# Kernel optimization log

Hardware: AMD Instinct MI355X
Metric: run time of the kernel (lower is better)

## Reference

```python
import jax, jax.numpy as jnp
import numpy as np

V, E, R, D, OUT, B = 50000, 400000, 400, 100, 200, 1024
EPS = 1e-5


def ccorr(a, b):
    # circular correlation: irfft(conj(rfft(a)) * rfft(b), n=D)
    return jnp.fft.irfft(jnp.conj(jnp.fft.rfft(a)) * jnp.fft.rfft(b), n=a.shape[-1]).astype(a.dtype)


def setup_inputs() -> dict:
    key = jax.random.key(0)
    ks = jax.random.split(key, 16)
    xav = lambda k, shp: jax.random.normal(k, shp, dtype=jnp.float32) * np.sqrt(2.0 / (shp[0] + shp[-1])) * np.sqrt(2.0)
    return {
        # graph / query (int constants)
        "edge_src": jax.random.randint(ks[0], (E,), 0, V, dtype=jnp.int32),
        "edge_dst": jax.random.randint(ks[1], (E,), 0, V, dtype=jnp.int32),
        "edge_type": jax.random.randint(ks[2], (E,), 0, R, dtype=jnp.int32),
        "head": jax.random.randint(ks[3], (B,), 0, V, dtype=jnp.int32),
        "rela": jax.random.randint(ks[4], (B,), 0, R, dtype=jnp.int32),
        "edge_norm": jax.random.uniform(ks[5], (E,), dtype=jnp.float32),
        # learned parameters
        "ent_emb": xav(ks[6], (V, D)),
        "rel_emb": xav(ks[7], (R, D)),
        "in_w": xav(ks[8], (D, OUT)),
        "out_w": xav(ks[9], (D, OUT)),
        "loop_w": xav(ks[10], (D, OUT)),
        "w_rel": xav(ks[11], (D, OUT)),
        "loop_rel": xav(ks[12], (1, D)),
        "conv_bias": jnp.zeros((OUT,), jnp.float32),
        "bn_gamma": jnp.ones((OUT,), jnp.float32),
        "bn_beta": jnp.zeros((OUT,), jnp.float32),
        "emb_ent": xav(ks[13], (V, OUT)),
        "ent_bias": jnp.zeros((V,), jnp.float32),
    }


def reference(edge_src, edge_dst, edge_type, head, rela, edge_norm,
              ent_emb, rel_emb, in_w, out_w, loop_w, w_rel, loop_rel,
              conv_bias, bn_gamma, bn_beta, emb_ent, ent_bias):
    # --- CompGCNCov (eval mode: dropouts are identity) ---
    h_src = ent_emb[edge_src]          # [E, D] gather
    r_e = rel_emb[edge_type]           # [E, D] gather
    edge_data = ccorr(h_src, r_e)      # [E, D] FFT compose (opn='corr')
    half = E // 2
    msg = jnp.concatenate([edge_data[:half] @ in_w, edge_data[half:] @ out_w])  # [E, OUT]
    msg = msg * edge_norm[:, None]
    agg = jax.ops.segment_sum(msg, edge_dst, num_segments=V) / 3.0             # scatter-sum + /3
    loop = ccorr(ent_emb, jnp.broadcast_to(loop_rel, ent_emb.shape)) @ loop_w / 3.0
    x = agg + loop + conv_bias
    # BatchNorm1d with batch statistics (training-mode stats, affine)
    mean = x.mean(axis=0)
    var = x.var(axis=0)
    x = (x - mean) / jnp.sqrt(var + EPS) * bn_gamma + bn_beta
    x = jnp.tanh(x)                    # act
    r_out = rel_emb @ w_rel            # [R, OUT]
    # --- DistMult decoder ---
    head_emb = x[head]                 # [B, OUT]
    rela_emb = r_out[rela]             # [B, OUT]
    obj = head_emb * rela_emb
    score = jax.nn.sigmoid(obj @ emb_ent.T + ent_bias)  # [B, V]
    return score
```

## Files before the change

### kernel.cpp

```cpp
#include <hip/hip_runtime.h>
#include <cstddef>

constexpr int V = 50000, E = 400000, R = 400, D = 100, OUT = 200, B = 1024;
constexpr int HALF = E / 2;
constexpr float EPS = 1e-5f;
constexpr int K2 = 232;
constexpr int VPAD = 50176;
constexpr int NKEY = 800;
constexpr int E1MAX = 450560;
constexpr int MT_O = 208, MT_K = 128;
constexpr int MT_SZ = MT_O * MT_K;
constexpr int NB2 = 196;
constexpr int BCAP = 2560;
constexpr int ECHK = 8;

typedef short bf16x8 __attribute__((ext_vector_type(8)));
typedef float f32x4  __attribute__((ext_vector_type(4)));
typedef unsigned short ushort8 __attribute__((ext_vector_type(8)));
typedef __attribute__((address_space(1))) const unsigned int guint_t;
typedef __attribute__((address_space(3))) unsigned int luint_t;

__device__ inline unsigned short f2bf(float x) {
    unsigned u = __float_as_uint(x);
    u = (u + 0x7fffu + ((u >> 16) & 1u)) >> 16;
    return (unsigned short)u;
}
__device__ inline float bf2f(unsigned short u) {
    return __uint_as_float(((unsigned)u) << 16);
}

constexpr int G_MLOOP = (D * OUT + 255) / 256;
constexpr int G_ROUT  = (R * OUT + 255) / 256;
constexpr int G_CVTWT = (2 * 208 * 16) / 256;
constexpr int G_CVTENT = (V * 16) / 256;
constexpr int PRE_B1 = G_MLOOP;
constexpr int PRE_B2 = PRE_B1 + G_ROUT;
constexpr int PRE_B3 = PRE_B2 + G_CVTWT;
constexpr int PRE_NWG = PRE_B3 + G_CVTENT;

__global__ __launch_bounds__(256) void k_pre(const float* __restrict__ loop_rel,
                                             const float* __restrict__ loop_w,
                                             const float* __restrict__ rel_emb,
                                             const float* __restrict__ w_rel,
                                             const float* __restrict__ in_w,
                                             const float* __restrict__ out_w,
                                             const float* __restrict__ ent_emb,
                                             float* __restrict__ Mloop,
                                             float* __restrict__ r_out,
                                             unsigned short* __restrict__ WT_bf,
                                             unsigned short* __restrict__ ent_bf) {
    int blk = blockIdx.x, t = threadIdx.x;
    if (blk < PRE_B1) {
        int i = blk * 256 + t;
        if (i >= D * OUT) return;
        int j = i / OUT, o = i % OUT;
        float s = 0.f;
        for (int k = 0; k < D; ++k) {
            int idx = j + k; if (idx >= D) idx -= D;
            s += loop_rel[idx] * loop_w[k * OUT + o];
        }
        Mloop[i] = s;
    } else if (blk < PRE_B2) {
        int i = (blk - PRE_B1) * 256 + t;
        if (i >= R * OUT) return;
        int r = i / OUT, o = i % OUT;
        float s = 0.f;
        for (int k = 0; k < D; ++k) s += rel_emb[r * D + k] * w_rel[k * OUT + o];
        r_out[i] = s;
    } else if (blk < PRE_B3) {
        int i = (blk - PRE_B2) * 256 + t;
        int side = i / (208 * 16);
        int rem = i - side * 208 * 16;
        int o = rem >> 4, c8 = rem & 15;
        int k0 = c8 * 8;
        const float* __restrict__ W = side ? out_w : in_w;
        ushort8 v = (ushort8)0;
        if (o < 200) {
#pragma unroll
            for (int q = 0; q < 8; ++q) {
                int k = k0 + q;
                if (k < 100) v[q] = f2bf(W[k * OUT + o]);
            }
        }
        *(ushort8*)&WT_bf[((size_t)side * 208 + o) * 128 + k0] = v;
    } else {
        int i = (blk - PRE_B3) * 256 + t;
        if (i >= V * 16) return;
        int v = i >> 4, c8 = i & 15;
        int c0 = c8 * 8;
        ushort8 o = (ushort8)0;
        if (c0 < 96) {
            float4 f0 = *(const float4*)&ent_emb[(size_t)v * D + c0];
            float4 f1 = *(const float4*)&ent_emb[(size_t)v * D + c0 + 4];
            o[0] = f2bf(f0.x); o[1] = f2bf(f0.y); o[2] = f2bf(f0.z); o[3] = f2bf(f0.w);
            o[4] = f2bf(f1.x); o[5] = f2bf(f1.y); o[6] = f2bf(f1.z); o[7] = f2bf(f1.w);
        } else if (c0 == 96) {
            float4 f0 = *(const float4*)&ent_emb[(size_t)v * D + 96];
            o[0] = f2bf(f0.x); o[1] = f2bf(f0.y); o[2] = f2bf(f0.z); o[3] = f2bf(f0.w);
        }
        *(ushort8*)&ent_bf[(size_t)v * 128 + c0] = o;
    }
}

__global__ __launch_bounds__(256) void k_hist(const int* __restrict__ etyp,
                                              int* __restrict__ hist1) {
    __shared__ int lh[NKEY];
    int t = threadIdx.x;
    for (int i = t; i < NKEY; i += 256) lh[i] = 0;
    __syncthreads();
    for (int e = blockIdx.x * 256 + t; e < E; e += gridDim.x * 256) {
        int key = etyp[e] + (e < HALF ? 0 : R);
        atomicAdd(&lh[key], 1);
    }
    __syncthreads();
    for (int i = t; i < NKEY; i += 256) {
        int c = lh[i];
        if (c) atomicAdd(&hist1[i], c);
    }
}

__global__ __launch_bounds__(1024) void k_scan(const int* __restrict__ hist1,
                                               int* __restrict__ start1,
                                               int* __restrict__ Edev) {
    __shared__ int buf[1024];
    int t = threadIdx.x;
    int c = (t < NKEY) ? ((hist1[t] + 63) & ~63) : 0;
    buf[t] = c; __syncthreads();
    for (int off = 1; off < 1024; off <<= 1) {
        int x = (t >= off) ? buf[t - off] : 0; __syncthreads();
        buf[t] += x; __syncthreads();
    }
    if (t < NKEY) start1[t] = buf[t] - c;
    if (t == NKEY - 1) { start1[NKEY] = buf[t]; *Edev = buf[t]; }
}

__global__ __launch_bounds__(1024) void k_binkey(const int* __restrict__ etyp,
                                                 const int* __restrict__ start1,
                                                 int* __restrict__ cursor1,
                                                 unsigned* __restrict__ perm1,
                                                 int* __restrict__ pos_of_e) {
    __shared__ int lhist[NKEY], lbase[NKEY], lcnt[NKEY];
    int t = threadIdx.x;
    int e0 = blockIdx.x * 8192;
    for (int i = t; i < NKEY; i += 1024) { lhist[i] = 0; lcnt[i] = 0; }
    __syncthreads();
    for (int i = t; i < 8192; i += 1024) {
        int e = e0 + i;
        if (e < E) {
            int key = etyp[e] + (e < HALF ? 0 : R);
            atomicAdd(&lhist[key], 1);
        }
    }
    __syncthreads();
    for (int i = t; i < NKEY; i += 1024) {
        int c = lhist[i];
        lbase[i] = c ? (start1[i] + atomicAdd(&cursor1[i], c)) : 0;
    }
    __syncthreads();
    for (int i = t; i < 8192; i += 1024) {
        int e = e0 + i;
        if (e < E) {
            int key = etyp[e] + (e < HALF ? 0 : R);
            int r = atomicAdd(&lcnt[key], 1);
            int p = lbase[key] + r;
            perm1[p] = (unsigned)e | ((unsigned)key << 19);
            pos_of_e[e] = p;
        }
    }
}

__global__ __launch_bounds__(1024) void k_bindst1(const int* __restrict__ edst,
                                                  const int* __restrict__ pos_of_e,
                                                  int* __restrict__ cursor196,
                                                  uint2* __restrict__ pairs) {
    __shared__ int chist[NB2], cbase[NB2], ccnt[NB2];
    int t = threadIdx.x;
    int e0 = blockIdx.x * 8192;
    for (int i = t; i < NB2; i += 1024) { chist[i] = 0; ccnt[i] = 0; }
    __syncthreads();
    for (int i = t; i < 8192; i += 1024) {
        int e = e0 + i;
        if (e < E) atomicAdd(&chist[edst[e] >> 8], 1);
    }
    __syncthreads();
    for (int i = t; i < NB2; i += 1024) {
        int c = chist[i];
        cbase[i] = c ? atomicAdd(&cursor196[i], c) : 0;
    }
    __syncthreads();
    for (int i = t; i < 8192; i += 1024) {
        int e = e0 + i;
        if (e < E) {
            int d = edst[e];
            int ld = d >> 8;
            int r = atomicAdd(&ccnt[ld], 1);
            int slot = cbase[ld] + r;
            if (slot < BCAP)
                pairs[(size_t)ld * BCAP + slot] = make_uint2((unsigned)d, (unsigned)pos_of_e[e]);
        }
    }
}

__global__ __launch_bounds__(256) void k_bindst2(const int* __restrict__ cursor196,
                                                 const uint2* __restrict__ pairs,
                                                 int* __restrict__ start2,
                                                 int* __restrict__ poslist) {
    __shared__ int lcnt[256], loff[256], lrk[256], bscan[256];
    int b = blockIdx.x, t = threadIdx.x;
    lcnt[t] = 0; lrk[t] = 0;
    bscan[t] = (t < NB2) ? min(cursor196[t], BCAP) : 0;
    __syncthreads();
    for (int off = 1; off < 256; off <<= 1) {
        int xx = (t >= off) ? bscan[t - off] : 0; __syncthreads();
        bscan[t] += xx; __syncthreads();
    }
    int base = (b > 0) ? bscan[b - 1] : 0;
    if (b == 0 && t == 0) start2[V] = bscan[NB2 - 1];
    int n = min(cursor196[b], BCAP);
    for (int i = t; i < n; i += 256) {
        int d = (int)pairs[(size_t)b * BCAP + i].x;
        atomicAdd(&lcnt[d - (b << 8)], 1);
    }
    __syncthreads();
    int cc = lcnt[t];
    loff[t] = cc; __syncthreads();
    for (int off = 1; off < 256; off <<= 1) {
        int xx = (t >= off) ? loff[t - off] : 0; __syncthreads();
        loff[t] += xx; __syncthreads();
    }
    int excl = loff[t] - cc;
    loff[t] = excl;
    int d = (b << 8) + t;
    if (d < V) start2[d] = base + excl;
    __syncthreads();
    for (int i = t; i < n; i += 256) {
        uint2 pr = pairs[(size_t)b * BCAP + i];
        int ld = (int)pr.x - (b << 8);
        int r = atomicAdd(&lrk[ld], 1);
        poslist[base + loff[ld] + r] = (int)pr.y;
    }
}

__global__ __launch_bounds__(256) void k_mtab(const float* __restrict__ rel_emb,
                                              const unsigned short* __restrict__ WT_bf,
                                              unsigned short* __restrict__ Mtab) {
    __shared__ unsigned short rsh[256];
    int key = blockIdx.x;
    int rho = (key < R) ? key : key - R;
    int side = (key < R) ? 0 : 1;
    int t = threadIdx.x, lane = t & 63, wid = t >> 6;
    {
        int sm = t;
        if (sm >= 200) sm -= 200; else if (sm >= 100) sm -= 100;
        rsh[t] = f2bf(rel_emb[rho * D + sm]);
    }
    __syncthreads();
    const unsigned short* WT = WT_bf + (size_t)side * 208 * 128;
    unsigned short* MtK = Mtab + (size_t)key * MT_SZ;
    int m16 = lane & 15, kq = lane >> 4;
    for (int jt = 0; jt < 2; ++jt) {
        int j0 = (wid * 2 + jt) * 16;
        f32x4 acc[13] = {};
        for (int ks = 0; ks < 4; ++ks) {
            int rbase = ks * 32 + kq * 8 + j0 + m16;
            ushort8 tmp;
#pragma unroll
            for (int q = 0; q < 8; ++q) tmp[q] = rsh[rbase + q];
            bf16x8 bfr = *(bf16x8*)&tmp;
#pragma unroll
            for (int of = 0; of < 13; ++of) {
                bf16x8 afr = *(const bf16x8*)&WT[(size_t)(of * 16 + m16) * 128 + ks * 32 + kq * 8];
                acc[of] = __builtin_amdgcn_mfma_f32_16x16x32_bf16(afr, bfr, acc[of], 0, 0, 0);
            }
        }
#pragma unroll
        for (int of = 0; of < 13; ++of) {
            int orow = of * 16 + kq * 4;
#pragma unroll
            for (int q = 0; q < 4; ++q)
                MtK[(size_t)(orow + q) * MT_K + j0 + m16] = f2bf(acc[of][q]);
        }
    }
}

__global__ __launch_bounds__(256, 2) void k_edgemm(const unsigned* __restrict__ perm1,
                                                   const int* __restrict__ Edev,
                                                   const int* __restrict__ esrc,
                                                   const float* __restrict__ enorm,
                                                   const unsigned short* __restrict__ ent_bf,
                                                   const unsigned short* __restrict__ Mtab,
                                                   unsigned short* __restrict__ msg) {
    __shared__ __align__(16) unsigned short MtL[MT_SZ];
    __shared__ __align__(16) unsigned short AtL[64 * MT_K];
    __shared__ float snrm[2][64];
    __shared__ int ssrc[2][64];
    int t = threadIdx.x, lane = t & 63, wid = t >> 6;
    int cpx = gridDim.x >> 3;
    int blk = (blockIdx.x & 7) * cpx + (blockIdx.x >> 3);
    int nE = *Edev;
    int curkey = -1;
    for (int c = 0; c < ECHK; ++c) {
        int chunk = blk * ECHK + c;
        if (chunk * 64 >= nE) break;
        int buf = c & 1;
        if (t < 64) {
            unsigned val = perm1[chunk * 64 + t];
            int e = (int)(val & 0x7FFFFu);
            bool ok = (val != 0xFFFFFFFFu);
            ssrc[buf][t] = ok ? esrc[e] : 0;
            snrm[buf][t] = ok ? enorm[e] : 0.f;
        }
        int key = (int)(perm1[chunk * 64] >> 19);
        __syncthreads();
        if (key != curkey) {
            for (int i = 0; i < 13; ++i) {
                int G0 = (wid * 13 + i) * 64;
                int G = G0 + lane;
                int o = G >> 4, g = G & 15;
                int gs = g ^ (o & 7);
                __builtin_amdgcn_global_load_lds(
                    (guint_t*)(Mtab + (size_t)key * MT_SZ + o * MT_K + gs * 8),
                    (luint_t*)(MtL + (size_t)G0 * 8), 16, 0, 0);
            }
            curkey = key;
        }
        for (int i = 0; i < 4; ++i) {
            int base = (wid * 4 + i) * 1024;
            int Gb = base + lane * 16;
            int row = Gb >> 8;
            int g = (Gb >> 4) & 15;
            int gs = g ^ (row & 7);
            __builtin_amdgcn_global_load_lds(
                (guint_t*)(ent_bf + (size_t)ssrc[buf][row] * 128 + gs * 8),
                (luint_t*)((char*)AtL + base), 16, 0, 0);
        }
        __syncthreads();
        int erow = wid * 16 + (lane & 15);
        int kq = lane >> 4;
        f32x4 acc[13] = {};
        for (int ks = 0; ks < 4; ++ks) {
            int g = ks * 4 + kq;
            bf16x8 bfr = *(const bf16x8*)((const char*)AtL + erow * 256 + ((g ^ (erow & 7)) * 16));
#pragma unroll
            for (int of = 0; of < 13; ++of) {
                int orow = of * 16 + (lane & 15);
                bf16x8 afr = *(const bf16x8*)((const char*)MtL + orow * 256 + ((g ^ (orow & 7)) * 16));
                acc[of] = __builtin_amdgcn_mfma_f32_16x16x32_bf16(afr, bfr, acc[of], 0, 0, 0);
            }
        }
        float nr = snrm[buf][erow];
        size_t rowbase = (size_t)(chunk * 64 + erow) * OUT;
#pragma unroll
        for (int of = 0; of < 13; ++of) {
            int o0 = of * 16 + kq * 4;
            if (o0 < OUT) {
                ushort4 pk;
                pk.x = f2bf(acc[of][0] * nr); pk.y = f2bf(acc[of][1] * nr);
                pk.z = f2bf(acc[of][2] * nr); pk.w = f2bf(acc[of][3] * nr);
                *(ushort4*)&msg[rowbase + o0] = pk;
            }
        }
    }
}

__global__ __launch_bounds__(256) void k_aggx(const int* __restrict__ start2,
                                              const int* __restrict__ poslist,
                                              const unsigned short* __restrict__ msg,
                                              const float* __restrict__ ent_emb,
                                              const float* __restrict__ Mloop,
                                              const float* __restrict__ conv_bias,
                                              float* __restrict__ x) {
    __shared__ float xt[16][200];
    __shared__ float sat[100][20];
    int t = threadIdx.x, lane = t & 63, wid = t >> 6;
    int v0 = blockIdx.x * 16;
    int half = (lane >= 25 && lane < 50) ? 1 : 0;
    int c = lane - half * 25;
    bool act = lane < 50;
    int src = lane + 25 < 64 ? lane + 25 : 63;
    for (int i = 0; i < 4; ++i) {
        int v = v0 + wid * 4 + i;
        int s = start2[v], epos = start2[v + 1];
        float acc[8] = {};
        for (int q = s; q < epos; q += 2) {
            int qq = q + half;
            if (act && qq < epos) {
                int p = poslist[qq];
                ushort8 m = *(const ushort8*)&msg[(size_t)p * OUT + c * 8];
#pragma unroll
                for (int j = 0; j < 8; ++j) acc[j] += bf2f(m[j]);
            }
        }
#pragma unroll
        for (int j = 0; j < 8; ++j) {
            float o = __shfl(acc[j], src);
            if (lane < 25) acc[j] += o;
        }
        if (lane < 25) {
#pragma unroll
            for (int j = 0; j < 8; ++j) xt[wid * 4 + i][lane * 8 + j] = acc[j];
        }
    }
    for (int i = t; i < 400; i += 256) {
        int kg = i >> 4, vv = i & 15;
        float4 a4 = *(const float4*)&ent_emb[(size_t)(v0 + vv) * D + kg * 4];
        sat[kg * 4 + 0][vv] = a4.x;
        sat[kg * 4 + 1][vv] = a4.y;
        sat[kg * 4 + 2][vv] = a4.z;
        sat[kg * 4 + 3][vv] = a4.w;
    }
    __syncthreads();
    if (t < 200) {
        int og = t % 50, eg = t / 50;
        int o0 = og * 4, vv0 = eg * 4;
        float acc[4][4] = {};
        for (int k = 0; k < D; ++k) {
            float4 w4 = *(const float4*)&Mloop[k * OUT + o0];
            float4 ca = *(const float4*)&sat[k][vv0];
            float cc[4] = {ca.x, ca.y, ca.z, ca.w};
            float wv[4] = {w4.x, w4.y, w4.z, w4.w};
#pragma unroll
            for (int r = 0; r < 4; ++r)
#pragma unroll
                for (int j = 0; j < 4; ++j) acc[r][j] += cc[r] * wv[j];
        }
        float4 bi = *(const float4*)&conv_bias[o0];
        float bv[4] = {bi.x, bi.y, bi.z, bi.w};
#pragma unroll
        for (int r = 0; r < 4; ++r) {
            int vv = vv0 + r;
            float4 ov;
            ov.x = (xt[vv][o0 + 0] + acc[r][0]) * (1.f / 3.f) + bv[0];
            ov.y = (xt[vv][o0 + 1] + acc[r][1]) * (1.f / 3.f) + bv[1];
            ov.z = (xt[vv][o0 + 2] + acc[r][2]) * (1.f / 3.f) + bv[2];
            ov.w = (xt[vv][o0 + 3] + acc[r][3]) * (1.f / 3.f) + bv[3];
            *(float4*)&x[(size_t)(v0 + vv) * OUT + o0] = ov;
        }
    }
}

__global__ __launch_bounds__(256) void k_stats(const float* __restrict__ x,
                                               float* __restrict__ colsum,
                                               float* __restrict__ colsq) {
    int g = blockIdx.x * 256 + threadIdx.x;
    int col = g % OUT;
    int r0 = g / OUT;
    float s = 0.f, sq = 0.f;
    for (int r = r0; r < V; r += 512) {
        float v = x[(size_t)r * OUT + col];
        s += v;
        sq += v * v;
    }
    atomicAdd(&colsum[col], s);
    atomicAdd(&colsq[col], sq);
}

__global__ __launch_bounds__(256) void k_obj(const int* __restrict__ head,
                                             const int* __restrict__ rela,
                                             const float* __restrict__ x,
                                             const float* __restrict__ colsum,
                                             const float* __restrict__ colsq,
                                             const float* __restrict__ gamma,
                                             const float* __restrict__ beta,
                                             const float* __restrict__ r_out,
                                             unsigned short* __restrict__ obj_bf) {
    int b = blockIdx.x, t = threadIdx.x;
    if (t >= K2) return;
    float v = 0.f;
    if (t < OUT) {
        float m = colsum[t] / (float)V;
        float var = colsq[t] / (float)V - m * m;
        float rs = rsqrtf(var + EPS);
        int h = head[b], r = rela[b];
        float val = (x[(size_t)h * OUT + t] - m) * rs * gamma[t] + beta[t];
        val = tanhf(val);
        v = val * r_out[r * OUT + t];
    }
    obj_bf[(size_t)b * K2 + t] = f2bf(v);
}

__global__ __launch_bounds__(256) void k_cvt_emb(const float* __restrict__ emb_ent,
                                                 unsigned short* __restrict__ emb_bf) {
    int i = blockIdx.x * 256 + threadIdx.x;
    if (i >= VPAD * 29) return;
    int v = i / 29, c8 = i % 29;
    int c0 = c8 * 8;
    ushort8 o = (ushort8)0;
    if (v < V && c0 < 200) {
        float4 f0 = *(const float4*)&emb_ent[(size_t)v * OUT + c0];
        float4 f1 = *(const float4*)&emb_ent[(size_t)v * OUT + c0 + 4];
        o[0] = f2bf(f0.x); o[1] = f2bf(f0.y); o[2] = f2bf(f0.z); o[3] = f2bf(f0.w);
        o[4] = f2bf(f1.x); o[5] = f2bf(f1.y); o[6] = f2bf(f1.z); o[7] = f2bf(f1.w);
    }
    *(ushort8*)&emb_bf[(size_t)v * K2 + c0] = o;
}

constexpr int DEC_BM = 64, DEC_BN = 256;
constexpr int DEC_GX = B / DEC_BM;
constexpr int DEC_GY = VPAD / DEC_BN;
constexpr int DEC_NWG = DEC_GX * DEC_GY;

__global__ __launch_bounds__(256) void k_dec2(const unsigned short* __restrict__ obj_bf,
                                              const unsigned short* __restrict__ emb_bf,
                                              const float* __restrict__ ent_bias,
                                              float* __restrict__ score) {
    int t = threadIdx.x;
    int lane = t & 63, wid = t >> 6;
    int wg = (blockIdx.x & 7) * (DEC_NWG >> 3) + (blockIdx.x >> 3);
    int b0 = (wg & (DEC_GX - 1)) * DEC_BM;
    int v0 = (wg >> 4) * DEC_BN;
    int r16 = lane & 15;
    int kc = (lane >> 4) * 8;
    int vbase = v0 + wid * 64;
    const unsigned short* gA = obj_bf + (size_t)(b0 + r16) * K2 + kc;
    const unsigned short* gB = emb_bf + (size_t)(vbase + r16) * K2 + kc;
    f32x4 acc[4][4] = {};
    for (int ks = 0; ks < 7; ++ks) {
        int kof = ks * 32;
        bf16x8 a[4], bb[4];
#pragma unroll
        for (int mf = 0; mf < 4; ++mf)
            a[mf] = *(const bf16x8*)(gA + (size_t)(mf * 16) * K2 + kof);
#pragma unroll
        for (int nf = 0; nf < 4; ++nf)
            bb[nf] = *(const bf16x8*)(gB + (size_t)(nf * 16) * K2 + kof);
#pragma unroll
        for (int mf = 0; mf < 4; ++mf)
#pragma unroll
            for (int nf = 0; nf < 4; ++nf)
                acc[mf][nf] = __builtin_amdgcn_mfma_f32_16x16x32_bf16(a[mf], bb[nf],
                                                                      acc[mf][nf], 0, 0, 0);
    }
#pragma unroll
    for (int nf = 0; nf < 4; ++nf) {
        int v = vbase + nf * 16 + r16;
        if (v >= V) continue;
        float bias = ent_bias[v];
#pragma unroll
        for (int mf = 0; mf < 4; ++mf) {
            int brow = b0 + mf * 16 + (lane >> 4) * 4;
            f32x4 av = acc[mf][nf];
#pragma unroll
            for (int i = 0; i < 4; ++i) {
                float val = av[i] + bias;
                score[(size_t)(brow + i) * V + v] = 1.f / (1.f + __expf(-val));
            }
        }
    }
}

extern "C" void kernel_launch(void* const* d_in, const int* in_sizes, int n_in,
                              void* d_out, int out_size, void* d_ws, size_t ws_size,
                              hipStream_t stream) {
    const int*   edge_src  = (const int*)d_in[0];
    const int*   edge_dst  = (const int*)d_in[1];
    const int*   edge_type = (const int*)d_in[2];
    const int*   head      = (const int*)d_in[3];
    const int*   rela      = (const int*)d_in[4];
    const float* edge_norm = (const float*)d_in[5];
    const float* ent_emb   = (const float*)d_in[6];
    const float* rel_emb   = (const float*)d_in[7];
    const float* in_w      = (const float*)d_in[8];
    const float* out_w     = (const float*)d_in[9];
    const float* loop_w    = (const float*)d_in[10];
    const float* w_rel     = (const float*)d_in[11];
    const float* loop_rel  = (const float*)d_in[12];
    const float* conv_bias = (const float*)d_in[13];
    const float* bn_gamma  = (const float*)d_in[14];
    const float* bn_beta   = (const float*)d_in[15];
    const float* emb_ent   = (const float*)d_in[16];
    const float* ent_bias  = (const float*)d_in[17];
    float* score = (float*)d_out;

    char* w = (char*)d_ws;
    float*          agg    = (float*)w;                      w += (size_t)V * OUT * 4;
    unsigned short* Mtab   = (unsigned short*)w;             w += (size_t)NKEY * MT_SZ * 2;
    unsigned*       perm1  = (unsigned*)w;                   w += (size_t)E1MAX * 4;
    int*            pos_of_e = (int*)w;                      w += (size_t)E * 4;
    int*            poslist  = (int*)w;                      w += (size_t)E * 4;
    uint2*          pairs    = (uint2*)w;                    w += (size_t)NB2 * BCAP * 8;
    char* zbase = w;
    int*   hist1     = (int*)w;                              w += NKEY * 4;
    int*   cursor1   = (int*)w;                              w += NKEY * 4;
    int*   cursor196 = (int*)w;                              w += NB2 * 4;
    float* colsum    = (float*)w;                            w += OUT * 4;
    float* colsq     = (float*)w;                            w += OUT * 4;
    size_t zbytes = (size_t)(w - zbase);
    int*   start1  = (int*)w;                                w += (NKEY + 1) * 4;
    int*   start2  = (int*)w;                                w += (V + 4) * 4;
    int*   Edev    = (int*)w;                                w += 16;
    float* Mloop   = (float*)w;                              w += (size_t)D * OUT * 4;
    float* r_out   = (float*)w;                              w += (size_t)R * OUT * 4;
    unsigned short* obj_bf = (unsigned short*)w;             w += (size_t)B * K2 * 2;
    unsigned short* WT_bf  = (unsigned short*)w;             w += (size_t)2 * 208 * 128 * 2;
    unsigned short* ent_bf = (unsigned short*)agg;
    unsigned short* emb_bf = (unsigned short*)agg;
    unsigned short* msg    = (unsigned short*)d_out;

    hipMemsetAsync(zbase, 0, zbytes, stream);
    hipMemsetAsync(perm1, 0xFF, (size_t)E1MAX * 4, stream);

    k_hist<<<512, 256, 0, stream>>>(edge_type, hist1);
    k_scan<<<1, 1024, 0, stream>>>(hist1, start1, Edev);
    k_binkey<<<(E + 8191) / 8192, 1024, 0, stream>>>(edge_type, start1, cursor1,
                                                     perm1, pos_of_e);
    k_bindst1<<<(E + 8191) / 8192, 1024, 0, stream>>>(edge_dst, pos_of_e, cursor196, pairs);
    k_bindst2<<<NB2, 256, 0, stream>>>(cursor196, pairs, start2, poslist);
    k_pre<<<PRE_NWG, 256, 0, stream>>>(loop_rel, loop_w, rel_emb, w_rel, in_w, out_w,
                                       ent_emb, Mloop, r_out, WT_bf, ent_bf);
    k_mtab<<<NKEY, 256, 0, stream>>>(rel_emb, WT_bf, Mtab);
    k_edgemm<<<E1MAX / 64 / ECHK, 256, 0, stream>>>(perm1, Edev, edge_src, edge_norm,
                                                    ent_bf, Mtab, msg);
    k_aggx<<<V / 16, 256, 0, stream>>>(start2, poslist, msg, ent_emb, Mloop,
                                       conv_bias, agg);
    k_stats<<<400, 256, 0, stream>>>(agg, colsum, colsq);
    k_obj<<<B, 256, 0, stream>>>(head, rela, agg, colsum, colsq, bn_gamma, bn_beta,
                                 r_out, obj_bf);
    k_cvt_emb<<<(VPAD * 29 + 255) / 256, 256, 0, stream>>>(emb_ent, emb_bf);
    k_dec2<<<DEC_NWG, 256, 0, stream>>>(obj_bf, emb_bf, ent_bias, score);
}
```

Measured before the change: 413.7 us.

## Fuse binning kernels, pad perm in scan, convert emb_ent inside decoder

Measured after the change: 488.3 us. 18.0% more time.

```diff
diff --git a/kernel.cpp b/kernel.cpp
--- a/kernel.cpp
+++ b/kernel.cpp
@@ -1,4 +1,5 @@
 #include <hip/hip_runtime.h>
+#include <hip/hip_bf16.h>
 #include <cstddef>
 
 constexpr int V = 50000, E = 400000, R = 400, D = 100, OUT = 200, B = 1024;
@@ -27,6 +28,16 @@
 }
 __device__ inline float bf2f(unsigned short u) {
     return __uint_as_float(((unsigned)u) << 16);
+}
+__device__ inline unsigned short f2bfh(float x) {
+    __hip_bfloat16 h = __float2bfloat16(x);
+    return *reinterpret_cast<unsigned short*>(&h);
+}
+__device__ inline bf16x8 pack8(float4 f0, float4 f1) {
+    union { bf16x8 v; unsigned short u[8]; } r;
+    r.u[0] = f2bfh(f0.x); r.u[1] = f2bfh(f0.y); r.u[2] = f2bfh(f0.z); r.u[3] = f2bfh(f0.w);
+    r.u[4] = f2bfh(f1.x); r.u[5] = f2bfh(f1.y); r.u[6] = f2bfh(f1.z); r.u[7] = f2bfh(f1.w);
+    return r.v;
 }
 
 constexpr int G_MLOOP = (D * OUT + 255) / 256;
@@ -121,40 +132,55 @@
 
 __global__ __launch_bounds__(1024) void k_scan(const int* __restrict__ hist1,
                                                int* __restrict__ start1,
-                                               int* __restrict__ Edev) {
+                                               int* __restrict__ Edev,
+                                               unsigned* __restrict__ perm1) {
     __shared__ int buf[1024];
     int t = threadIdx.x;
-    int c = (t < NKEY) ? ((hist1[t] + 63) & ~63) : 0;
+    int h = (t < NKEY) ? hist1[t] : 0;
+    int c = (h + 63) & ~63;
     buf[t] = c; __syncthreads();
     for (int off = 1; off < 1024; off <<= 1) {
         int x = (t >= off) ? buf[t - off] : 0; __syncthreads();
         buf[t] += x; __syncthreads();
     }
-    if (t < NKEY) start1[t] = buf[t] - c;
+    int s = buf[t] - c;
+    if (t < NKEY) {
+        start1[t] = s;
+        for (int i = h; i < c; ++i) perm1[s + i] = 0xFFFFFFFFu;
+    }
     if (t == NKEY - 1) { start1[NKEY] = buf[t]; *Edev = buf[t]; }
 }
 
-__global__ __launch_bounds__(1024) void k_binkey(const int* __restrict__ etyp,
-                                                 const int* __restrict__ start1,
-                                                 int* __restrict__ cursor1,
-                                                 unsigned* __restrict__ perm1,
-                                                 int* __restrict__ pos_of_e) {
+__global__ __launch_bounds__(1024) void k_bin(const int* __restrict__ etyp,
+                                              const int* __restrict__ edst,
+                                              const int* __restrict__ start1,
+                                              int* __restrict__ cursor1,
+                                              int* __restrict__ cursor196,
+                                              unsigned* __restrict__ perm1,
+                                              uint2* __restrict__ pairs) {
     __shared__ int lhist[NKEY], lbase[NKEY], lcnt[NKEY];
+    __shared__ int chist[NB2], cbase[NB2], ccnt[NB2];
     int t = threadIdx.x;
     int e0 = blockIdx.x * 8192;
     for (int i = t; i < NKEY; i += 1024) { lhist[i] = 0; lcnt[i] = 0; }
+    for (int i = t; i < NB2; i += 1024) { chist[i] = 0; ccnt[i] = 0; }
     __syncthreads();
     for (int i = t; i < 8192; i += 1024) {
         int e = e0 + i;
         if (e < E) {
             int key = etyp[e] + (e < HALF ? 0 : R);
             atomicAdd(&lhist[key], 1);
+            atomicAdd(&chist[edst[e] >> 8], 1);
         }
     }
     __syncthreads();
     for (int i = t; i < NKEY; i += 1024) {
         int c = lhist[i];
         lbase[i] = c ? (start1[i] + atomicAdd(&cursor1[i], c)) : 0;
+    }
+    for (int i = t; i < NB2; i += 1024) {
+        int c = chist[i];
+        cbase[i] = c ? atomicAdd(&cursor196[i], c) : 0;
     }
     __syncthreads();
     for (int i = t; i < 8192; i += 1024) {
@@ -164,39 +190,12 @@
             int r = atomicAdd(&lcnt[key], 1);
             int p = lbase[key] + r;
             perm1[p] = (unsigned)e | ((unsigned)key << 19);
-            pos_of_e[e] = p;
-        }
-    }
-}
-
-__global__ __launch_bounds__(1024) void k_bindst1(const int* __restrict__ edst,
-                                                  const int* __restrict__ pos_of_e,
-                                                  int* __restrict__ cursor196,
-                                                  uint2* __restrict__ pairs) {
-    __shared__ int chist[NB2], cbase[NB2], ccnt[NB2];
-    int t = threadIdx.x;
-    int e0 = blockIdx.x * 8192;
-    for (int i = t; i < NB2; i += 1024) { chist[i] = 0; ccnt[i] = 0; }
-    __syncthreads();
-    for (int i = t; i < 8192; i += 1024) {
-        int e = e0 + i;
-        if (e < E) atomicAdd(&chist[edst[e] >> 8], 1);
-    }
-    __syncthreads();
-    for (int i = t; i < NB2; i += 1024) {
-        int c = chist[i];
-        cbase[i] = c ? atomicAdd(&cursor196[i], c) : 0;
-    }
-    __syncthreads();
-    for (int i = t; i < 8192; i += 1024) {
-        int e = e0 + i;
-        if (e < E) {
             int d = edst[e];
             int ld = d >> 8;
-            int r = atomicAdd(&ccnt[ld], 1);
-            int slot = cbase[ld] + r;
+            int rr = atomicAdd(&ccnt[ld], 1);
+            int slot = cbase[ld] + rr;
             if (slot < BCAP)
-                pairs[(size_t)ld * BCAP + slot] = make_uint2((unsigned)d, (unsigned)pos_of_e[e]);
+                pairs[(size_t)ld * BCAP + slot] = make_uint2((unsigned)d, (unsigned)p);
         }
     }
 }
@@ -479,29 +478,13 @@
     obj_bf[(size_t)b * K2 + t] = f2bf(v);
 }
 
-__global__ __launch_bounds__(256) void k_cvt_emb(const float* __restrict__ emb_ent,
-                                                 unsigned short* __restrict__ emb_bf) {
-    int i = blockIdx.x * 256 + threadIdx.x;
-    if (i >= VPAD * 29) return;
-    int v = i / 29, c8 = i % 29;
-    int c0 = c8 * 8;
-    ushort8 o = (ushort8)0;
-    if (v < V && c0 < 200) {
-        float4 f0 = *(const float4*)&emb_ent[(size_t)v * OUT + c0];
-        float4 f1 = *(const float4*)&emb_ent[(size_t)v * OUT + c0 + 4];
-        o[0] = f2bf(f0.x); o[1] = f2bf(f0.y); o[2] = f2bf(f0.z); o[3] = f2bf(f0.w);
-        o[4] = f2bf(f1.x); o[5] = f2bf(f1.y); o[6] = f2bf(f1.z); o[7] = f2bf(f1.w);
-    }
-    *(ushort8*)&emb_bf[(size_t)v * K2 + c0] = o;
-}
-
 constexpr int DEC_BM = 64, DEC_BN = 256;
 constexpr int DEC_GX = B / DEC_BM;
 constexpr int DEC_GY = VPAD / DEC_BN;
 constexpr int DEC_NWG = DEC_GX * DEC_GY;
 
 __global__ __launch_bounds__(256) void k_dec2(const unsigned short* __restrict__ obj_bf,
-                                              const unsigned short* __restrict__ emb_bf,
+                                              const float* __restrict__ emb_ent,
                                               const float* __restrict__ ent_bias,
                                               float* __restrict__ score) {
     int t = threadIdx.x;
@@ -510,20 +493,52 @@
     int b0 = (wg & (DEC_GX - 1)) * DEC_BM;
     int v0 = (wg >> 4) * DEC_BN;
     int r16 = lane & 15;
-    int kc = (lane >> 4) * 8;
+    int kq = lane >> 4;
+    int kc = kq * 8;
     int vbase = v0 + wid * 64;
     const unsigned short* gA = obj_bf + (size_t)(b0 + r16) * K2 + kc;
-    const unsigned short* gB = emb_bf + (size_t)(vbase + r16) * K2 + kc;
+    const float* gB[4];
+#pragma unroll
+    for (int nf = 0; nf < 4; ++nf) {
+        int vr = min(vbase + nf * 16 + r16, V - 1);
+        gB[nf] = emb_ent + (size_t)vr * OUT + kc;
+    }
     f32x4 acc[4][4] = {};
-    for (int ks = 0; ks < 7; ++ks) {
+    for (int ks = 0; ks < 6; ++ks) {
         int kof = ks * 32;
         bf16x8 a[4], bb[4];
 #pragma unroll
         for (int mf = 0; mf < 4; ++mf)
             a[mf] = *(const bf16x8*)(gA + (size_t)(mf * 16) * K2 + kof);
 #pragma unroll
-        for (int nf = 0; nf < 4; ++nf)
-            bb[nf] = *(const bf16x8*)(gB + (size_t)(nf * 16) * K2 + kof);
+        for (int nf = 0; nf < 4; ++nf) {
+            float4 f0 = *(const float4*)(gB[nf] + kof);
+            float4 f1 = *(const float4*)(gB[nf] + kof + 4);
+            bb[nf] = pack8(f0, f1);
+        }
+#pragma unroll
+        for (int mf = 0; mf < 4; ++mf)
+#pragma unroll
+            for (int nf = 0; nf < 4; ++nf)
+                acc[mf][nf] = __builtin_amdgcn_mfma_f32_16x16x32_bf16(a[mf], bb[nf],
+                                                                      acc[mf][nf], 0, 0, 0);
+    }
+    {
+        bf16x8 a[4], bb[4];
+#pragma unroll
+        for (int mf = 0; mf < 4; ++mf)
+            a[mf] = *(const bf16x8*)(gA + (size_t)(mf * 16) * K2 + 192);
+        if (kq == 0) {
+#pragma unroll
+            for (int nf = 0; nf < 4; ++nf) {
+                float4 f0 = *(const float4*)(gB[nf] + 192);
+                float4 f1 = *(const float4*)(gB[nf] + 196);
+                bb[nf] = pack8(f0, f1);
+            }
+        } else {
+#pragma unroll
+            for (int nf = 0; nf < 4; ++nf) bb[nf] = (bf16x8)0;
+        }
 #pragma unroll
         for (int mf = 0; mf < 4; ++mf)
 #pragma unroll
@@ -538,7 +553,7 @@
         float bias = ent_bias[v];
 #pragma unroll
         for (int mf = 0; mf < 4; ++mf) {
-            int brow = b0 + mf * 16 + (lane >> 4) * 4;
+            int brow = b0 + mf * 16 + kq * 4;
             f32x4 av = acc[mf][nf];
 #pragma unroll
             for (int i = 0; i < 4; ++i) {
@@ -576,7 +591,6 @@
     float*          agg    = (float*)w;                      w += (size_t)V * OUT * 4;
     unsigned short* Mtab   = (unsigned short*)w;             w += (size_t)NKEY * MT_SZ * 2;
     unsigned*       perm1  = (unsigned*)w;                   w += (size_t)E1MAX * 4;
-    int*            pos_of_e = (int*)w;                      w += (size_t)E * 4;
     int*            poslist  = (int*)w;                      w += (size_t)E * 4;
     uint2*          pairs    = (uint2*)w;                    w += (size_t)NB2 * BCAP * 8;
     char* zbase = w;
@@ -594,17 +608,14 @@
     unsigned short* obj_bf = (unsigned short*)w;             w += (size_t)B * K2 * 2;
     unsigned short* WT_bf  = (unsigned short*)w;             w += (size_t)2 * 208 * 128 * 2;
     unsigned short* ent_bf = (unsigned short*)agg;
-    unsigned short* emb_bf = (unsigned short*)agg;
     unsigned short* msg    = (unsigned short*)d_out;
 
     hipMemsetAsync(zbase, 0, zbytes, stream);
-    hipMemsetAsync(perm1, 0xFF, (size_t)E1MAX * 4, stream);
 
     k_hist<<<512, 256, 0, stream>>>(edge_type, hist1);
-    k_scan<<<1, 1024, 0, stream>>>(hist1, start1, Edev);
-    k_binkey<<<(E + 8191) / 8192, 1024, 0, stream>>>(edge_type, start1, cursor1,
-                                                     perm1, pos_of_e);
-    k_bindst1<<<(E + 8191) / 8192, 1024, 0, stream>>>(edge_dst, pos_of_e, cursor196, pairs);
+    k_scan<<<1, 1024, 0, stream>>>(hist1, start1, Edev, perm1);
+    k_bin<<<(E + 8191) / 8192, 1024, 0, stream>>>(edge_type, edge_dst, start1,
+                                                  cursor1, cursor196, perm1, pairs);
     k_bindst2<<<NB2, 256, 0, stream>>>(cursor196, pairs, start2, poslist);
     k_pre<<<PRE_NWG, 256, 0, stream>>>(loop_rel, loop_w, rel_emb, w_rel, in_w, out_w,
                                        ent_emb, Mloop, r_out, WT_bf, ent_bf);
@@ -616,6 +627,5 @@
     k_stats<<<400, 256, 0, stream>>>(agg, colsum, colsq);
     k_obj<<<B, 256, 0, stream>>>(head, rela, agg, colsum, colsq, bn_gamma, bn_beta,
                                  r_out, obj_bf);
-    k_cvt_emb<<<(VPAD * 29 + 255) / 256, 256, 0, stream>>>(emb_ent, emb_bf);
-    k_dec2<<<DEC_NWG, 256, 0, stream>>>(obj_bf, emb_bf, ent_bias, score);
-}
+    k_dec2<<<DEC_NWG, 256, 0, stream>>>(obj_bf, emb_ent, ent_bias, score);
+}
```
